# Optimization experiments

Measured on AMD Instinct MI355X. Metric: run time of the kernel, lower is better.

Reference implementation:

```python
import jax, jax.numpy as jnp
import numpy as np

IN_F, OUT_F = 4096, 16384
ACT_IN, ACT_OUT = 2048, 8192
B, S = 4, 2048


def setup_inputs() -> dict:
    key = jax.random.key(0)
    k1, k2, k3 = jax.random.split(key, 3)
    rng = np.random.default_rng(0)
    in_idx = jnp.asarray(np.sort(rng.choice(IN_F, size=ACT_IN, replace=False)), dtype=jnp.int32)
    out_idx = jnp.asarray(np.sort(rng.choice(OUT_F, size=ACT_OUT, replace=False)), dtype=jnp.int32)
    x = jax.random.normal(k1, (B, S, IN_F), dtype=jnp.float32)
    # nn.Linear init scale ~ 1/sqrt(fan_in)
    weight = jax.random.normal(k2, (ACT_OUT, ACT_IN), dtype=jnp.float32) / np.sqrt(ACT_IN)
    bias = jax.random.normal(k3, (ACT_OUT,), dtype=jnp.float32) / np.sqrt(ACT_IN)
    return {"x": x, "weight": weight, "bias": bias, "in_indices": in_idx, "out_indices": out_idx}


def reference(x, weight, bias, in_indices, out_indices):
    batch_dims = x.shape[:-1]
    x_flat = x.reshape(-1, IN_F)                      # [N, in_f]
    x_active = x_flat[:, in_indices]                  # gather cols -> [N, act_in]
    y_active = jnp.einsum('ni,oi->no', x_active, weight) + bias  # [N, act_out]
    out_flat = jnp.zeros((x_flat.shape[0], OUT_F), dtype=y_active.dtype)
    out_flat = out_flat.at[:, out_indices].set(y_active)  # scatter cols
    return out_flat.reshape(batch_dims + (OUT_F,))
```

## Files before the change

kernel.cpp:

```cpp
#include <hip/hip_runtime.h>
#include <stdint.h>

#define IN_F    4096
#define OUT_F   16384
#define ACT_IN  2048
#define ACT_OUT 8192
#define NROWS   8192

typedef __bf16 bf16;
typedef __bf16 bf16x8 __attribute__((ext_vector_type(8)));
typedef float  f32x4  __attribute__((ext_vector_type(4)));

#define BM 128
#define BN 128
#define BK 32

__device__ __forceinline__ void g2lds16(const void* g, void* l) {
  __builtin_amdgcn_global_load_lds(
      (const __attribute__((address_space(1))) void*)(uintptr_t)g,
      (__attribute__((address_space(3))) void*)(uint32_t)(uintptr_t)l,
      16, 0, 0);
}

__global__ void zero_out_kernel(float* __restrict__ out) {
  size_t i = ((size_t)blockIdx.x * blockDim.x + threadIdx.x) * 4;
  f32x4 z = {0.f, 0.f, 0.f, 0.f};
  *reinterpret_cast<f32x4*>(out + i) = z;
}

__global__ void gather_cast_x(const float* __restrict__ x,
                              const int* __restrict__ in_idx,
                              bf16* __restrict__ A) {
  int n  = blockIdx.x;
  int k0 = threadIdx.x << 3;
  const float* xr = x + (size_t)n * IN_F;
  bf16x8 v;
#pragma unroll
  for (int j = 0; j < 8; ++j) v[j] = (bf16)xr[in_idx[k0 + j]];
  *reinterpret_cast<bf16x8*>(A + (size_t)n * ACT_IN + k0) = v;
}

__global__ void cast_w_kernel(const float* __restrict__ w, bf16* __restrict__ W) {
  size_t base = ((size_t)blockIdx.x * blockDim.x + threadIdx.x) * 8;
  float4 f0 = *reinterpret_cast<const float4*>(w + base);
  float4 f1 = *reinterpret_cast<const float4*>(w + base + 4);
  bf16x8 v;
  v[0] = (bf16)f0.x; v[1] = (bf16)f0.y; v[2] = (bf16)f0.z; v[3] = (bf16)f0.w;
  v[4] = (bf16)f1.x; v[5] = (bf16)f1.y; v[6] = (bf16)f1.z; v[7] = (bf16)f1.w;
  *reinterpret_cast<bf16x8*>(W + base) = v;
}

__global__ __launch_bounds__(256, 2)
void gemm_scatter(const bf16* __restrict__ A,
                  const bf16* __restrict__ W,
                  const float* __restrict__ bias,
                  const int* __restrict__ out_idx,
                  float* __restrict__ out) {
  __shared__ bf16 As[BM * BK];
  __shared__ bf16 Bs[BN * BK];

  const int tid  = threadIdx.x;
  const int lane = tid & 63;
  const int quad = lane >> 4;
  const int l16  = lane & 15;
  const int wave = tid >> 6;
  const int wm   = (wave & 1) << 6;
  const int wn   = (wave >> 1) << 6;
  const int m0   = blockIdx.y * BM;
  const int n0   = blockIdx.x * BN;

  const int se   = tid << 3;
  const int srow = se >> 5;
  const int scol = se & 31;
  const bf16* Ag0 = A + (size_t)(m0 + srow) * ACT_IN + scol;
  const bf16* Ag1 = Ag0 + (size_t)64 * ACT_IN;
  const bf16* Bg0 = W + (size_t)(n0 + srow) * ACT_IN + scol;
  const bf16* Bg1 = Bg0 + (size_t)64 * ACT_IN;
  bf16* lA0 = As + se;
  bf16* lA1 = As + 64 * BK + se;
  bf16* lB0 = Bs + se;
  bf16* lB1 = Bs + 64 * BK + se;

  f32x4 acc[4][4] = {};

  for (int k0 = 0; k0 < ACT_IN; k0 += BK) {
    g2lds16(Ag0 + k0, lA0);
    g2lds16(Ag1 + k0, lA1);
    g2lds16(Bg0 + k0, lB0);
    g2lds16(Bg1 + k0, lB1);
    __syncthreads();

    bf16x8 af[4], bfr[4];
#pragma unroll
    for (int i = 0; i < 4; ++i)
      af[i] = *reinterpret_cast<const bf16x8*>(As + (wm + i * 16 + l16) * BK + quad * 8);
#pragma unroll
    for (int j = 0; j < 4; ++j)
      bfr[j] = *reinterpret_cast<const bf16x8*>(Bs + (wn + j * 16 + l16) * BK + quad * 8);

#pragma unroll
    for (int i = 0; i < 4; ++i)
#pragma unroll
      for (int j = 0; j < 4; ++j)
        acc[i][j] = __builtin_amdgcn_mfma_f32_16x16x32_bf16(af[i], bfr[j], acc[i][j], 0, 0, 0);

    __syncthreads();
  }

#pragma unroll
  for (int j = 0; j < 4; ++j) {
    const int col = n0 + wn + j * 16 + l16;
    const int oc  = out_idx[col];
    const float b = bias[col];
#pragma unroll
    for (int i = 0; i < 4; ++i) {
      const int row = m0 + wm + i * 16 + (quad << 2);
#pragma unroll
      for (int r = 0; r < 4; ++r)
        out[(size_t)(row + r) * OUT_F + oc] = acc[i][j][r] + b;
    }
  }
}

extern "C" void kernel_launch(void* const* d_in, const int* in_sizes, int n_in,
                              void* d_out, int out_size, void* d_ws, size_t ws_size,
                              hipStream_t stream) {
  const float* x       = (const float*)d_in[0];
  const float* w       = (const float*)d_in[1];
  const float* bias    = (const float*)d_in[2];
  const int*   in_idx  = (const int*)d_in[3];
  const int*   out_idx = (const int*)d_in[4];
  float* out = (float*)d_out;

  bf16* A  = (bf16*)d_ws;
  bf16* Wb = (bf16*)((char*)d_ws + (size_t)NROWS * ACT_IN * 2);

  {
    size_t n4 = (size_t)out_size / 4;
    zero_out_kernel<<<(uint32_t)(n4 / 256), 256, 0, stream>>>(out);
  }
  gather_cast_x<<<NROWS, 256, 0, stream>>>(x, in_idx, A);
  cast_w_kernel<<<(ACT_OUT * (size_t)ACT_IN / 8) / 256, 256, 0, stream>>>(w, Wb);
  gemm_scatter<<<dim3(ACT_OUT / BN, NROWS / BM), 256, 0, stream>>>(A, Wb, bias, out_idx, out);
}
```

Baseline: 1.104 ms.

## Fuse output zero-fill into GEMM epilogue via LDS-staged coalesced scatter

Removes the separate kernel that zero-fills the full output and instead has each GEMM block write every output column between its neighbouring active indices, filling inactive columns with zeros. Accumulators are staged through a padded LDS tile, and a per-chunk column map turns the strided scattered stores into contiguous row writes. The gather kernel also loads its eight indices as two vector loads. The cost is extra barriers and LDS traffic in the epilogue, plus a correctness dependence on out_idx being sorted so that the column ranges tile the output exactly.

Measured after the change: 1.025 ms. -7.1%, faster.

```diff
diff --git a/kernel.cpp b/kernel.cpp
--- a/kernel.cpp
+++ b/kernel.cpp
@@ -14,6 +14,8 @@
 #define BM 128
 #define BN 128
 #define BK 32
+#define TSTRIDE 34
+#define CMAX 64
 
 __device__ __forceinline__ void g2lds16(const void* g, void* l) {
   __builtin_amdgcn_global_load_lds(
@@ -22,21 +24,19 @@
       16, 0, 0);
 }
 
-__global__ void zero_out_kernel(float* __restrict__ out) {
-  size_t i = ((size_t)blockIdx.x * blockDim.x + threadIdx.x) * 4;
-  f32x4 z = {0.f, 0.f, 0.f, 0.f};
-  *reinterpret_cast<f32x4*>(out + i) = z;
-}
-
 __global__ void gather_cast_x(const float* __restrict__ x,
                               const int* __restrict__ in_idx,
                               bf16* __restrict__ A) {
   int n  = blockIdx.x;
   int k0 = threadIdx.x << 3;
   const float* xr = x + (size_t)n * IN_F;
+  int4 i0 = *reinterpret_cast<const int4*>(in_idx + k0);
+  int4 i1 = *reinterpret_cast<const int4*>(in_idx + k0 + 4);
   bf16x8 v;
-#pragma unroll
-  for (int j = 0; j < 8; ++j) v[j] = (bf16)xr[in_idx[k0 + j]];
+  v[0] = (bf16)xr[i0.x]; v[1] = (bf16)xr[i0.y];
+  v[2] = (bf16)xr[i0.z]; v[3] = (bf16)xr[i0.w];
+  v[4] = (bf16)xr[i1.x]; v[5] = (bf16)xr[i1.y];
+  v[6] = (bf16)xr[i1.z]; v[7] = (bf16)xr[i1.w];
   *reinterpret_cast<bf16x8*>(A + (size_t)n * ACT_IN + k0) = v;
 }
 
@@ -56,8 +56,11 @@
                   const float* __restrict__ bias,
                   const int* __restrict__ out_idx,
                   float* __restrict__ out) {
-  __shared__ bf16 As[BM * BK];
-  __shared__ bf16 Bs[BN * BK];
+  __shared__ __align__(16) char smraw[128 * TSTRIDE * 4 + CMAX * 4];
+  bf16* As = (bf16*)smraw;
+  bf16* Bs = (bf16*)(smraw + BM * BK * 2);
+  float* tile = (float*)smraw;
+  int*   cmap = (int*)(smraw + 128 * TSTRIDE * 4);
 
   const int tid  = threadIdx.x;
   const int lane = tid & 63;
@@ -107,17 +110,49 @@
     __syncthreads();
   }
 
+  for (int cc = 0; cc < 4; ++cc) {
+    __syncthreads();
+    if ((cc >> 1) == (wn >> 6)) {
 #pragma unroll
-  for (int j = 0; j < 4; ++j) {
-    const int col = n0 + wn + j * 16 + l16;
-    const int oc  = out_idx[col];
-    const float b = bias[col];
+      for (int jj = 0; jj < 2; ++jj) {
+        const int j  = ((cc & 1) << 1) + jj;
+        const int cl = (jj << 4) + l16;
+        const float bv = bias[n0 + wn + j * 16 + l16];
 #pragma unroll
-    for (int i = 0; i < 4; ++i) {
-      const int row = m0 + wm + i * 16 + (quad << 2);
+        for (int i = 0; i < 4; ++i) {
+          const int rb = wm + i * 16 + (quad << 2);
 #pragma unroll
-      for (int r = 0; r < 4; ++r)
-        out[(size_t)(row + r) * OUT_F + oc] = acc[i][j][r] + b;
+          for (int r = 0; r < 4; ++r)
+            tile[(rb + r) * TSTRIDE + cl] = acc[i][j][r] + bv;
+        }
+      }
+    }
+
+    const int a0   = n0 + cc * 32;
+    const int lo   = (a0 == 0) ? 0 : out_idx[a0 - 1] + 1;
+    const int aend = out_idx[a0 + 31];
+    const int hi   = (a0 + 31 == ACT_OUT - 1) ? OUT_F - 1 : aend;
+
+    for (int base = lo; base <= hi; base += CMAX) {
+      int wd = hi - base + 1; if (wd > CMAX) wd = CMAX;
+      __syncthreads();
+      if (tid < CMAX) cmap[tid] = -1;
+      __syncthreads();
+      if (tid < 32) {
+        int rel = out_idx[a0 + tid] - base;
+        if (rel >= 0 && rel < CMAX) cmap[rel] = tid;
+      }
+      __syncthreads();
+      const int lc = tid & 63;
+      if (lc < wd) {
+        const int cm = cmap[lc];
+        size_t ob = (size_t)(m0 + wave * 32) * OUT_F + base + lc;
+#pragma unroll 4
+        for (int r = 0; r < 32; ++r) {
+          float v = (cm >= 0) ? tile[(wave * 32 + r) * TSTRIDE + cm] : 0.0f;
+          out[ob + (size_t)r * OUT_F] = v;
+        }
+      }
     }
   }
 }
@@ -135,10 +170,6 @@
   bf16* A  = (bf16*)d_ws;
   bf16* Wb = (bf16*)((char*)d_ws + (size_t)NROWS * ACT_IN * 2);
 
-  {
-    size_t n4 = (size_t)out_size / 4;
-    zero_out_kernel<<<(uint32_t)(n4 / 256), 256, 0, stream>>>(out);
-  }
   gather_cast_x<<<NROWS, 256, 0, stream>>>(x, in_idx, A);
   cast_w_kernel<<<(ACT_OUT * (size_t)ACT_IN / 8) / 256, 256, 0, stream>>>(w, Wb);
   gemm_scatter<<<dim3(ACT_OUT / BN, NROWS / BM), 256, 0, stream>>>(A, Wb, bias, out_idx, out);
```
